# Kernel tuning notes

Measured on AMD Instinct MI355X. Metric: run time of the kernel, lower is better.

Reference implementation:

```python
import jax, jax.numpy as jnp
import numpy as np

# Module hyperparameters (from init_kwargs)
INPUT_SIZE = 1024
OUTPUT_SIZE = 1024
ORDER = 3
GRID_RANGE = (-1.0, 1.0)
GRID_COUNT = 8
CENTER_COUNT = GRID_COUNT + ORDER + 1  # 12

_lo, _hi = GRID_RANGE
_end_center = _hi + (_hi - _lo) * (ORDER + 1) / (GRID_COUNT - 1)
CENTERS = jnp.asarray(np.linspace(_lo, _end_center, CENTER_COUNT), dtype=jnp.float32)
ZOOM = (_hi - _lo) / 2.0
PAN = (_hi + _lo) / 2.0


def setup_inputs() -> dict:
    key = jax.random.key(0)
    k1, k2 = jax.random.split(key)
    x = jax.random.normal(k1, (4096, INPUT_SIZE), dtype=jnp.float32)
    coef = jax.random.normal(k2, (OUTPUT_SIZE, INPUT_SIZE, GRID_COUNT), dtype=jnp.float32) * 0.1
    return {"x": x, "coef": coef}


def _spline_basis(x):
    # x: [B, I] -> basis: [B, I, GRID_COUNT] via Cox-de Boor recursion
    xt = jnp.tanh(x) * ZOOM + PAN
    c = CENTERS
    xe = xt[..., None]  # [B, I, 1]
    # order-0: indicator of [c[i], c[i+1]) for i = 0..CENTER_COUNT-2
    b = ((xe >= c[:-1]) & (xe < c[1:])).astype(xt.dtype)  # [B, I, CENTER_COUNT-1]
    for k in range(1, ORDER + 1):
        n = CENTER_COUNT - k - 1
        c0, ck = c[:n], c[k:k + n]
        c1, ck1 = c[1:n + 1], c[k + 1:k + 1 + n]
        left = (xe - c0) / (ck - c0)          # [B, I, n]
        right = (ck1 - xe) / (ck1 - c1)       # [B, I, n]
        b = left * b[..., :n] + right * b[..., 1:n + 1]
    return b  # [B, I, GRID_COUNT]


def reference(x, coef):
    spline = _spline_basis(x)                      # [B, I, G]
    # sum_j over inputs of coef-weighted basis: [B, O]
    return jnp.einsum('big,oig->bo', spline, coef)
```

## Files before the change

### kernel.cpp

```cpp
#include <hip/hip_runtime.h>
#include <stdint.h>
#include <stddef.h>


#define BATCH 4096
#define IN    1024
#define OUTN  1024
#define KDIM  (IN * 8)
#define NTT   (KDIM / 64)

typedef __attribute__((ext_vector_type(8)))  short          short8;
typedef __attribute__((ext_vector_type(8)))  unsigned short ushort8;
typedef __attribute__((ext_vector_type(4)))  float          f32x4;


__device__ __forceinline__ constexpr float Cf(int i) {
    constexpr double end  = 1.0 + 2.0 * 4.0 / 7.0;
    constexpr double step = (end - (-1.0)) / 11.0;
    return (float)(-1.0 + (double)i * step);
}

__device__ __forceinline__ unsigned short f2bf(float f) {
    unsigned int u = __builtin_bit_cast(unsigned int, f);
    u += 0x7fffu + ((u >> 16) & 1u);
    return (unsigned short)(u >> 16);
}

__device__ __forceinline__ float bf2f(unsigned short u) {
    unsigned int v = (unsigned int)u << 16;
    return __builtin_bit_cast(float, v);
}

__device__ __forceinline__ ushort8 spline8(float xt) {
    float v[11];
#pragma unroll
    for (int j = 0; j < 11; ++j)
        v[j] = (xt >= Cf(j) && xt < Cf(j + 1)) ? 1.0f : 0.0f;
#pragma unroll
    for (int k = 1; k <= 3; ++k) {
#pragma unroll
        for (int j = 0; j < 11 - k; ++j) {
            float left  = (xt - Cf(j))         * (1.0f / (Cf(j + k)     - Cf(j)));
            float right = (Cf(j + k + 1) - xt) * (1.0f / (Cf(j + k + 1) - Cf(j + 1)));
            v[j] = left * v[j] + right * v[j + 1];
        }
    }
    ushort8 r;
#pragma unroll
    for (int g = 0; g < 8; ++g) r[g] = f2bf(v[g]);
    return r;
}

typedef const unsigned int __attribute__((address_space(1))) gu32;
typedef unsigned int       __attribute__((address_space(3))) lu32;

__device__ __forceinline__ void gload_lds16(const void* g, void* l) {
    __builtin_amdgcn_global_load_lds((gu32*)g, (lu32*)l, 16, 0, 0);
}


__global__ void prep_kernel(const float* __restrict__ x, const float* __restrict__ coef,
                            unsigned short* __restrict__ A, unsigned short* __restrict__ B) {
    const int t = threadIdx.x;
    int blk = blockIdx.x;
    if (blk < 4096) {
        const int bb = blk >> 4, bi = blk & 15;
        const int b  = bb * 16 + (t & 15);
        const int i0 = bi * 64 + (t >> 4) * 4;
        f32x4 xv = *reinterpret_cast<const f32x4*>(&x[(size_t)b * IN + i0]);
        ushort8 r[4];
#pragma unroll
        for (int j = 0; j < 4; ++j) r[j] = spline8(tanhf(xv[j]));
        ushort8* out = reinterpret_cast<ushort8*>(A)
                     + ((size_t)(bb * 256 + bi * 16 + (t >> 4)) * 64) + (t & 15);
        out[0]  = r[0];
        out[16] = r[1];
        out[32] = r[2];
        out[48] = r[3];
    } else {
        blk -= 4096;
        const int ob = blk >> 4, ib = blk & 15;
        const int oo = ob * 16 + (t & 15);
        const int i0 = ib * 64 + (t >> 4) * 4;
        const f32x4* cin = reinterpret_cast<const f32x4*>(coef);
        ushort8 r[4];
#pragma unroll
        for (int j = 0; j < 4; ++j) {
            f32x4 v0 = cin[((size_t)oo * IN + i0 + j) * 2];
            f32x4 v1 = cin[((size_t)oo * IN + i0 + j) * 2 + 1];
#pragma unroll
            for (int g = 0; g < 4; ++g) { r[j][g] = f2bf(v0[g]); r[j][4 + g] = f2bf(v1[g]); }
        }
        ushort8* out = reinterpret_cast<ushort8*>(B)
                     + ((size_t)(ob * 256 + ib * 16 + (t >> 4)) * 64) + (t & 15);
        out[0]  = r[0];
        out[16] = r[1];
        out[32] = r[2];
        out[48] = r[3];
    }
}


#define LSA0 (&Ls[0][0])
#define LSB0 (&Ls[0][16384])
#define LSA1 (&Ls[1][0])
#define LSB1 (&Ls[1][16384])

template<int NSPLIT>
__global__ __launch_bounds__(512, 2) void gemm_bt(
        const unsigned short* __restrict__ Ashuf,
        const unsigned short* __restrict__ Bshuf,
        float* __restrict__ C,
        unsigned short* __restrict__ P) {
    constexpr int NT2 = NTT / NSPLIT;
    static_assert((NT2 & 1) == 0, "loop assumes even NT2");
    __shared__ unsigned short Ls[2][32768];

    const int tid  = threadIdx.x;
    const int w    = tid >> 6;
    const int lane = tid & 63;
    const int wm   = w >> 2, wn = w & 3;
    const int kkw  = w & 1, wh = w >> 1;
    const int lane8 = lane * 8;

    const int bid  = blockIdx.x;
    const int s    = bid & (NSPLIT - 1);
    const int tile = bid / NSPLIT;
    const int mb16 = (tile >> 2) * 16;
    const int nb16 = (tile & 3) * 16;
    const int T0   = s * NT2;
    const int brow = mb16 * 16, bcol = nb16 * 16;

#define STAGE_OP(BASE, NB16, H, T, LS) do {                                   \
        size_t _kq = ((size_t)(2 * (T0 + (T)) + kkw)) * 512 + lane8;          \
        const unsigned short* _g = (BASE) + ((size_t)((NB16) + (H)*8 + wh) << 17) + _kq; \
        unsigned short* _l = (LS) + (((H)*16 + w) << 9);                      \
        gload_lds16(_g, _l);                                                  \
        gload_lds16(_g + ((size_t)4 << 17), _l + (8 << 9));                   \
    } while (0)
#define STAGE_A(H, T, LS) STAGE_OP(Ashuf, mb16, H, T, LS)
#define STAGE_B(H, T, LS) STAGE_OP(Bshuf, nb16, H, T, LS)

#define LDA_F(DST, H, LS) do {                                                \
        _Pragma("unroll")                                                     \
        for (int mf = 0; mf < 4; ++mf)                                        \
            _Pragma("unroll")                                                 \
            for (int kk = 0; kk < 2; ++kk)                                    \
                DST[mf][kk] = *reinterpret_cast<const short8*>(               \
                    (LS) + (((((H)*8 + wm*4 + mf) * 2) + kk) << 9) + lane8);  \
    } while (0)
#define LDB_F(DST, V, LS) do {                                                \
        _Pragma("unroll")                                                     \
        for (int nf = 0; nf < 2; ++nf)                                        \
            _Pragma("unroll")                                                 \
            for (int kk = 0; kk < 2; ++kk)                                    \
                DST[nf][kk] = *reinterpret_cast<const short8*>(               \
                    (LS) + (((((V)*8 + wn*2 + nf) * 2) + kk) << 9) + lane8);  \
    } while (0)

    f32x4 acc[8][4] = {};
    short8 aF[4][2], bv0[2][2], bv1[2][2];

#define MFMA_Q(H, V, AF, BV) do {                                             \
        __builtin_amdgcn_s_setprio(1);                                        \
        _Pragma("unroll")                                                     \
        for (int kk = 0; kk < 2; ++kk)                                        \
            _Pragma("unroll")                                                 \
            for (int mf = 0; mf < 4; ++mf)                                    \
                _Pragma("unroll")                                             \
                for (int nf = 0; nf < 2; ++nf)                                \
                    acc[(H)*4 + mf][(V)*2 + nf] =                             \
                        __builtin_amdgcn_mfma_f32_16x16x32_bf16(              \
                            AF[mf][kk], BV[nf][kk],                           \
                            acc[(H)*4 + mf][(V)*2 + nf], 0, 0, 0);            \
        __builtin_amdgcn_s_setprio(0);                                        \
    } while (0)

#define TILE(T, LAC, LBC, LAN, LBN, S1F, S23F, RN, VC) do {                   \
        __builtin_amdgcn_s_barrier();                                         \
        MFMA_Q(0, 0, aF, bv0);                                                \
        LDB_F(bv1, 1, LBC);                                                   \
        if (S1F) { STAGE_B(1, (T) + 1, LBN); STAGE_A(1, (T) + 1, LAN); }      \
        __builtin_amdgcn_s_barrier();                                         \
        MFMA_Q(0, 1, aF, bv1);                                                \
        LDA_F(aF, 1, LAC);                                                    \
        if (S23F) STAGE_B(0, (T) + 2, LBC);                                   \
        __builtin_amdgcn_s_barrier();                                         \
        MFMA_Q(1, 0, aF, bv0);                                                \
        if (S23F) STAGE_A(0, (T) + 2, LAC);                                   \
        asm volatile("s_waitcnt vmcnt(" VC ")" ::: "memory");                 \
        __builtin_amdgcn_s_barrier();                                         \
        MFMA_Q(1, 1, aF, bv1);                                                \
        if (RN) { LDA_F(aF, 0, LAN); LDB_F(bv0, 0, LBN); }                    \
    } while (0)

    STAGE_B(0, 0, LSB0); STAGE_A(0, 0, LSA0);
    STAGE_B(1, 0, LSB0); STAGE_A(1, 0, LSA0);
    STAGE_B(0, 1, LSB1); STAGE_A(0, 1, LSA1);
    asm volatile("s_waitcnt vmcnt(4)" ::: "memory");
    __builtin_amdgcn_s_barrier();
    LDA_F(aF, 0, LSA0); LDB_F(bv0, 0, LSB0);

#pragma unroll 1
    for (int t = 0; t + 2 <= NT2 - 2; t += 2) {
        TILE(t,     LSA0, LSB0, LSA1, LSB1, 1, 1, 1, "4");
        TILE(t + 1, LSA1, LSB1, LSA0, LSB0, 1, 1, 1, "4");
    }
    TILE(NT2 - 2, LSA0, LSB0, LSA1, LSB1, 1, 0, 1, "0");
    TILE(NT2 - 1, LSA1, LSB1, LSA0, LSB0, 0, 0, 0, "0");

    const int q4 = (lane >> 4) * 4, frow = lane & 15;
    if (NSPLIT == 1 || s == 0) {
#pragma unroll
        for (int H = 0; H < 2; ++H)
#pragma unroll
            for (int mf = 0; mf < 4; ++mf)
#pragma unroll
                for (int V = 0; V < 2; ++V)
#pragma unroll
                    for (int nf = 0; nf < 2; ++nf)
#pragma unroll
                        for (int r = 0; r < 4; ++r) {
                            int row = brow + H * 128 + wm * 64 + mf * 16 + q4 + r;
                            int col = bcol + V * 128 + wn * 32 + nf * 16 + frow;
                            C[(size_t)row * OUTN + col] = acc[H * 4 + mf][V * 2 + nf][r];
                        }
    } else {
        unsigned short* Pb = P + (size_t)(s - 1) * BATCH * OUTN;
#pragma unroll
        for (int H = 0; H < 2; ++H)
#pragma unroll
            for (int mf = 0; mf < 4; ++mf)
#pragma unroll
                for (int V = 0; V < 2; ++V)
#pragma unroll
                    for (int nf = 0; nf < 2; ++nf)
#pragma unroll
                        for (int r = 0; r < 4; ++r) {
                            int row = brow + H * 128 + wm * 64 + mf * 16 + q4 + r;
                            int col = bcol + V * 128 + wn * 32 + nf * 16 + frow;
                            Pb[(size_t)row * OUTN + col] = f2bf(acc[H * 4 + mf][V * 2 + nf][r]);
                        }
    }
}


__global__ void reduce_kernel(float* __restrict__ C, const unsigned short* __restrict__ P,
                              int np) {
    int i = blockIdx.x * 256 + threadIdx.x;
    size_t base = (size_t)i * 8;
    f32x4 c0 = *reinterpret_cast<f32x4*>(&C[base]);
    f32x4 c1 = *reinterpret_cast<f32x4*>(&C[base + 4]);
    for (int j = 0; j < np; ++j) {
        ushort8 p = *reinterpret_cast<const ushort8*>(&P[(size_t)j * BATCH * OUTN + base]);
#pragma unroll
        for (int e = 0; e < 4; ++e) c0[e] += bf2f(p[e]);
#pragma unroll
        for (int e = 0; e < 4; ++e) c1[e] += bf2f(p[4 + e]);
    }
    *reinterpret_cast<f32x4*>(&C[base])     = c0;
    *reinterpret_cast<f32x4*>(&C[base + 4]) = c1;
}


extern "C" void kernel_launch(void* const* d_in, const int* in_sizes, int n_in,
                              void* d_out, int out_size, void* d_ws, size_t ws_size,
                              hipStream_t stream) {
    const float* x    = (const float*)d_in[0];
    const float* coef = (const float*)d_in[1];
    float* out = (float*)d_out;

    unsigned short* ashuf = (unsigned short*)d_ws;
    unsigned short* bshuf = ashuf + (size_t)BATCH * KDIM;
    unsigned short* part  = bshuf + (size_t)OUTN * KDIM;
    const size_t base = (size_t)BATCH * KDIM * 2 + (size_t)OUTN * KDIM * 2;
    const size_t slab = (size_t)BATCH * OUTN * 2;

    prep_kernel<<<5120, 256, 0, stream>>>(x, coef, ashuf, bshuf);

    if (ws_size >= base + 3 * slab) {
        gemm_bt<4><<<256, 512, 0, stream>>>(ashuf, bshuf, out, part);
        reduce_kernel<<<2048, 256, 0, stream>>>(out, part, 3);
    } else if (ws_size >= base + slab) {
        gemm_bt<2><<<128, 512, 0, stream>>>(ashuf, bshuf, out, part);
        reduce_kernel<<<2048, 256, 0, stream>>>(out, part, 1);
    } else {
        gemm_bt<1><<<64, 512, 0, stream>>>(ashuf, bshuf, out, nullptr);
    }
}
```

Before: 96.43 us.

## Restructure GEMM to 256-thread blocks with triple-buffered K=32 pipeline

Reworks the bf16 MFMA GEMM so each block is 256 threads computing a 256x128 output tile instead of 512 threads on 256x256. The K loop now advances in 32-wide steps with a three-stage LDS ring buffer, replacing the 64-wide double buffer. This doubles the grid to 512 blocks so more blocks can be resident on the CUs, and it simplifies the staging and barrier schedule. In exchange each block reuses less B data per load and needs more barriers per unit of K. The NSPLIT=2 fallback path is also removed.

```diff
diff --git a/kernel.cpp b/kernel.cpp
--- a/kernel.cpp
+++ b/kernel.cpp
@@ -7,7 +7,7 @@
 #define IN    1024
 #define OUTN  1024
 #define KDIM  (IN * 8)
-#define NTT   (KDIM / 64)
+#define NSTEP (KDIM / 32)
 
 typedef __attribute__((ext_vector_type(8)))  short          short8;
 typedef __attribute__((ext_vector_type(8)))  unsigned short ushort8;
@@ -101,146 +101,135 @@
 }
 
 
-#define LSA0 (&Ls[0][0])
-#define LSB0 (&Ls[0][16384])
-#define LSA1 (&Ls[1][0])
-#define LSB1 (&Ls[1][16384])
-
 template<int NSPLIT>
-__global__ __launch_bounds__(512, 2) void gemm_bt(
+__global__ __launch_bounds__(256, 2) void gemm_bt(
         const unsigned short* __restrict__ Ashuf,
         const unsigned short* __restrict__ Bshuf,
         float* __restrict__ C,
         unsigned short* __restrict__ P) {
-    constexpr int NT2 = NTT / NSPLIT;
-    static_assert((NT2 & 1) == 0, "loop assumes even NT2");
-    __shared__ unsigned short Ls[2][32768];
+    constexpr int NT2 = NSTEP / NSPLIT;
+    static_assert(NT2 >= 8 && (NT2 - 4) % 3 == 0, "tail assumes (NT2-4)%3==0");
+    __shared__ unsigned short Ls[3][12288];
 
     const int tid  = threadIdx.x;
     const int w    = tid >> 6;
     const int lane = tid & 63;
-    const int wm   = w >> 2, wn = w & 3;
-    const int kkw  = w & 1, wh = w >> 1;
+    const int wm   = w >> 1, wn = w & 1;
     const int lane8 = lane * 8;
+    const int w4 = w * 4, w2 = w * 2;
 
     const int bid  = blockIdx.x;
-    const int s    = bid & (NSPLIT - 1);
-    const int tile = bid / NSPLIT;
-    const int mb16 = (tile >> 2) * 16;
-    const int nb16 = (tile & 3) * 16;
+    const int s    = (NSPLIT == 1) ? 0 : (bid & (NSPLIT - 1));
+    const int tile = (NSPLIT == 1) ? bid : (bid / NSPLIT);
+    const int tm   = tile >> 3;
+    const int tn   = tile & 7;
+    const int mb16 = tm * 16;
+    const int nb8  = tn * 8;
     const int T0   = s * NT2;
-    const int brow = mb16 * 16, bcol = nb16 * 16;
-
-#define STAGE_OP(BASE, NB16, H, T, LS) do {                                   \
-        size_t _kq = ((size_t)(2 * (T0 + (T)) + kkw)) * 512 + lane8;          \
-        const unsigned short* _g = (BASE) + ((size_t)((NB16) + (H)*8 + wh) << 17) + _kq; \
-        unsigned short* _l = (LS) + (((H)*16 + w) << 9);                      \
-        gload_lds16(_g, _l);                                                  \
-        gload_lds16(_g + ((size_t)4 << 17), _l + (8 << 9));                   \
-    } while (0)
-#define STAGE_A(H, T, LS) STAGE_OP(Ashuf, mb16, H, T, LS)
-#define STAGE_B(H, T, LS) STAGE_OP(Bshuf, nb16, H, T, LS)
-
-#define LDA_F(DST, H, LS) do {                                                \
+    const int brow = tm * 256, bcol = tn * 128;
+
+#define STAGE(T2, LS) do {                                                    \
+        size_t _kq = (size_t)(T0 + (T2)) * 512 + lane8;                       \
+        _Pragma("unroll")                                                     \
+        for (int j = 0; j < 4; ++j)                                           \
+            gload_lds16(Ashuf + (((size_t)(mb16 + w4 + j)) << 17) + _kq,      \
+                        (LS) + (w4 + j) * 512);                               \
+        _Pragma("unroll")                                                     \
+        for (int j = 0; j < 2; ++j)                                           \
+            gload_lds16(Bshuf + (((size_t)(nb8 + w2 + j)) << 17) + _kq,       \
+                        (LS) + 8192 + (w2 + j) * 512);                        \
+    } while (0)
+
+#define LDA_LO(LS) do {                                                      \
+        _Pragma("unroll")                                                    \
+        for (int mf = 0; mf < 4; ++mf)                                       \
+            aF[mf] = *reinterpret_cast<const short8*>(                       \
+                (LS) + (wm * 8 + mf) * 512 + lane8);                         \
+    } while (0)
+#define LDA_HI(LS) do {                                                     \
+        _Pragma("unroll")                                                    \
+        for (int mf = 0; mf < 4; ++mf)                                       \
+            aF[4 + mf] = *reinterpret_cast<const short8*>(                   \
+                (LS) + (wm * 8 + 4 + mf) * 512 + lane8);                     \
+    } while (0)
+#define LDB(LS) do {                                                         \
+        _Pragma("unroll")                                                    \
+        for (int nf = 0; nf < 4; ++nf)                                       \
+            bv[nf] = *reinterpret_cast<const short8*>(                       \
+                (LS) + 8192 + (wn * 4 + nf) * 512 + lane8);                  \
+    } while (0)
+
+    f32x4 acc[8][4] = {};
+    short8 aF[8], bv[4];
+
+#define MFMA_HALF(L) do {                                                     \
+        __builtin_amdgcn_s_setprio(1);                                        \
         _Pragma("unroll")                                                     \
         for (int mf = 0; mf < 4; ++mf)                                        \
             _Pragma("unroll")                                                 \
-            for (int kk = 0; kk < 2; ++kk)                                    \
-                DST[mf][kk] = *reinterpret_cast<const short8*>(               \
-                    (LS) + (((((H)*8 + wm*4 + mf) * 2) + kk) << 9) + lane8);  \
-    } while (0)
-#define LDB_F(DST, V, LS) do {                                                \
-        _Pragma("unroll")                                                     \
-        for (int nf = 0; nf < 2; ++nf)                                        \
-            _Pragma("unroll")                                                 \
-            for (int kk = 0; kk < 2; ++kk)                                    \
-                DST[nf][kk] = *reinterpret_cast<const short8*>(               \
-                    (LS) + (((((V)*8 + wn*2 + nf) * 2) + kk) << 9) + lane8);  \
-    } while (0)
-
-    f32x4 acc[8][4] = {};
-    short8 aF[4][2], bv0[2][2], bv1[2][2];
-
-#define MFMA_Q(H, V, AF, BV) do {                                             \
-        __builtin_amdgcn_s_setprio(1);                                        \
-        _Pragma("unroll")                                                     \
-        for (int kk = 0; kk < 2; ++kk)                                        \
-            _Pragma("unroll")                                                 \
-            for (int mf = 0; mf < 4; ++mf)                                    \
-                _Pragma("unroll")                                             \
-                for (int nf = 0; nf < 2; ++nf)                                \
-                    acc[(H)*4 + mf][(V)*2 + nf] =                             \
-                        __builtin_amdgcn_mfma_f32_16x16x32_bf16(              \
-                            AF[mf][kk], BV[nf][kk],                           \
-                            acc[(H)*4 + mf][(V)*2 + nf], 0, 0, 0);            \
+            for (int nf = 0; nf < 4; ++nf)                                    \
+                acc[(L)*4 + mf][nf] =                                         \
+                    __builtin_amdgcn_mfma_f32_16x16x32_bf16(                  \
+                        aF[(L)*4 + mf], bv[nf], acc[(L)*4 + mf][nf], 0, 0, 0);\
         __builtin_amdgcn_s_setprio(0);                                        \
     } while (0)
 
-#define TILE(T, LAC, LBC, LAN, LBN, S1F, S23F, RN, VC) do {                   \
+#define STEP(T, CUR, NXT, STG, SFLAG, VC, RN) do {                            \
         __builtin_amdgcn_s_barrier();                                         \
-        MFMA_Q(0, 0, aF, bv0);                                                \
-        LDB_F(bv1, 1, LBC);                                                   \
-        if (S1F) { STAGE_B(1, (T) + 1, LBN); STAGE_A(1, (T) + 1, LAN); }      \
-        __builtin_amdgcn_s_barrier();                                         \
-        MFMA_Q(0, 1, aF, bv1);                                                \
-        LDA_F(aF, 1, LAC);                                                    \
-        if (S23F) STAGE_B(0, (T) + 2, LBC);                                   \
-        __builtin_amdgcn_s_barrier();                                         \
-        MFMA_Q(1, 0, aF, bv0);                                                \
-        if (S23F) STAGE_A(0, (T) + 2, LAC);                                   \
+        if (SFLAG) STAGE((T) + 2, STG);                                       \
+        MFMA_HALF(0);                                                         \
+        LDA_HI(CUR);                                                          \
         asm volatile("s_waitcnt vmcnt(" VC ")" ::: "memory");                 \
         __builtin_amdgcn_s_barrier();                                         \
-        MFMA_Q(1, 1, aF, bv1);                                                \
-        if (RN) { LDA_F(aF, 0, LAN); LDB_F(bv0, 0, LBN); }                    \
-    } while (0)
-
-    STAGE_B(0, 0, LSB0); STAGE_A(0, 0, LSA0);
-    STAGE_B(1, 0, LSB0); STAGE_A(1, 0, LSA0);
-    STAGE_B(0, 1, LSB1); STAGE_A(0, 1, LSA1);
-    asm volatile("s_waitcnt vmcnt(4)" ::: "memory");
+        MFMA_HALF(1);                                                         \
+        if (RN) { LDA_LO(NXT); LDB(NXT); }                                    \
+    } while (0)
+
+    unsigned short* b0 = &Ls[0][0];
+    unsigned short* b1 = &Ls[1][0];
+    unsigned short* b2 = &Ls[2][0];
+
+    STAGE(0, b0);
+    STAGE(1, b1);
+    asm volatile("s_waitcnt vmcnt(6)" ::: "memory");
     __builtin_amdgcn_s_barrier();
-    LDA_F(aF, 0, LSA0); LDB_F(bv0, 0, LSB0);
+    LDA_LO(b0); LDB(b0);
 
 #pragma unroll 1
-    for (int t = 0; t + 2 <= NT2 - 2; t += 2) {
-        TILE(t,     LSA0, LSB0, LSA1, LSB1, 1, 1, 1, "4");
-        TILE(t + 1, LSA1, LSB1, LSA0, LSB0, 1, 1, 1, "4");
-    }
-    TILE(NT2 - 2, LSA0, LSB0, LSA1, LSB1, 1, 0, 1, "0");
-    TILE(NT2 - 1, LSA1, LSB1, LSA0, LSB0, 0, 0, 0, "0");
+    for (int t = 0; t < NT2 - 4; t += 3) {
+        STEP(t,     b0, b1, b2, 1, "6", 1);
+        STEP(t + 1, b1, b2, b0, 1, "6", 1);
+        STEP(t + 2, b2, b0, b1, 1, "6", 1);
+    }
+    STEP(NT2 - 4, b0, b1, b2, 1, "6", 1);
+    STEP(NT2 - 3, b1, b2, b0, 1, "6", 1);
+    STEP(NT2 - 2, b2, b0, b1, 0, "0", 1);
+    STEP(NT2 - 1, b0, b1, b2, 0, "0", 0);
 
     const int q4 = (lane >> 4) * 4, frow = lane & 15;
     if (NSPLIT == 1 || s == 0) {
 #pragma unroll
-        for (int H = 0; H < 2; ++H)
-#pragma unroll
-            for (int mf = 0; mf < 4; ++mf)
-#pragma unroll
-                for (int V = 0; V < 2; ++V)
-#pragma unroll
-                    for (int nf = 0; nf < 2; ++nf)
-#pragma unroll
-                        for (int r = 0; r < 4; ++r) {
-                            int row = brow + H * 128 + wm * 64 + mf * 16 + q4 + r;
-                            int col = bcol + V * 128 + wn * 32 + nf * 16 + frow;
-                            C[(size_t)row * OUTN + col] = acc[H * 4 + mf][V * 2 + nf][r];
-                        }
+        for (int mf = 0; mf < 8; ++mf)
+#pragma unroll
+            for (int nf = 0; nf < 4; ++nf)
+#pragma unroll
+                for (int r = 0; r < 4; ++r) {
+                    int row = brow + wm * 128 + mf * 16 + q4 + r;
+                    int col = bcol + wn * 64 + nf * 16 + frow;
+                    C[(size_t)row * OUTN + col] = acc[mf][nf][r];
+                }
     } else {
         unsigned short* Pb = P + (size_t)(s - 1) * BATCH * OUTN;
 #pragma unroll
-        for (int H = 0; H < 2; ++H)
-#pragma unroll
-            for (int mf = 0; mf < 4; ++mf)
-#pragma unroll
-                for (int V = 0; V < 2; ++V)
-#pragma unroll
-                    for (int nf = 0; nf < 2; ++nf)
-#pragma unroll
-                        for (int r = 0; r < 4; ++r) {
-                            int row = brow + H * 128 + wm * 64 + mf * 16 + q4 + r;
-                            int col = bcol + V * 128 + wn * 32 + nf * 16 + frow;
-                            Pb[(size_t)row * OUTN + col] = f2bf(acc[H * 4 + mf][V * 2 + nf][r]);
-                        }
+        for (int mf = 0; mf < 8; ++mf)
+#pragma unroll
+            for (int nf = 0; nf < 4; ++nf)
+#pragma unroll
+                for (int r = 0; r < 4; ++r) {
+                    int row = brow + wm * 128 + mf * 16 + q4 + r;
+                    int col = bcol + wn * 64 + nf * 16 + frow;
+                    Pb[(size_t)row * OUTN + col] = f2bf(acc[mf][nf][r]);
+                }
     }
 }
 
@@ -279,12 +268,9 @@
     prep_kernel<<<5120, 256, 0, stream>>>(x, coef, ashuf, bshuf);
 
     if (ws_size >= base + 3 * slab) {
-        gemm_bt<4><<<256, 512, 0, stream>>>(ashuf, bshuf, out, part);
+        gemm_bt<4><<<512, 256, 0, stream>>>(ashuf, bshuf, out, part);
         reduce_kernel<<<2048, 256, 0, stream>>>(out, part, 3);
-    } else if (ws_size >= base + slab) {
-        gemm_bt<2><<<128, 512, 0, stream>>>(ashuf, bshuf, out, part);
-        reduce_kernel<<<2048, 256, 0, stream>>>(out, part, 1);
     } else {
-        gemm_bt<1><<<64, 512, 0, stream>>>(ashuf, bshuf, out, nullptr);
-    }
-}
+        gemm_bt<1><<<128, 256, 0, stream>>>(ashuf, bshuf, out, nullptr);
+    }
+}
```

Measured after the change: 101.8 us. +5.6%, slower.

## Load B fragments directly from global memory, stage only A in LDS

Applied to the files above, without the earlier changes.

The GEMM kernel stops staging the B operand through shared memory. Each wave now loads its B fragments straight from global memory into registers, and LDS holds only double-buffered A tiles, halving shared memory use. The pipeline schedule and waitcnt counts are reworked to match. This removes LDS write/read traffic for B and may allow more resident blocks, but B is now fetched redundantly across waves with exposed global latency.

```diff
diff --git a/kernel.cpp b/kernel.cpp
--- a/kernel.cpp
+++ b/kernel.cpp
@@ -102,9 +102,7 @@
 
 
 #define LSA0 (&Ls[0][0])
-#define LSB0 (&Ls[0][16384])
 #define LSA1 (&Ls[1][0])
-#define LSB1 (&Ls[1][16384])
 
 template<int NSPLIT>
 __global__ __launch_bounds__(512, 2) void gemm_bt(
@@ -113,8 +111,8 @@
         float* __restrict__ C,
         unsigned short* __restrict__ P) {
     constexpr int NT2 = NTT / NSPLIT;
-    static_assert((NT2 & 1) == 0, "loop assumes even NT2");
-    __shared__ unsigned short Ls[2][32768];
+    static_assert((NT2 & 1) == 0 && NT2 >= 8, "loop assumes even NT2 >= 8");
+    __shared__ unsigned short Ls[2][16384];
 
     const int tid  = threadIdx.x;
     const int w    = tid >> 6;
@@ -131,15 +129,13 @@
     const int T0   = s * NT2;
     const int brow = mb16 * 16, bcol = nb16 * 16;
 
-#define STAGE_OP(BASE, NB16, H, T, LS) do {                                   \
+#define STAGE_A(H, T, LS) do {                                                \
         size_t _kq = ((size_t)(2 * (T0 + (T)) + kkw)) * 512 + lane8;          \
-        const unsigned short* _g = (BASE) + ((size_t)((NB16) + (H)*8 + wh) << 17) + _kq; \
+        const unsigned short* _g = Ashuf + ((size_t)(mb16 + (H)*8 + wh) << 17) + _kq; \
         unsigned short* _l = (LS) + (((H)*16 + w) << 9);                      \
         gload_lds16(_g, _l);                                                  \
         gload_lds16(_g + ((size_t)4 << 17), _l + (8 << 9));                   \
     } while (0)
-#define STAGE_A(H, T, LS) STAGE_OP(Ashuf, mb16, H, T, LS)
-#define STAGE_B(H, T, LS) STAGE_OP(Bshuf, nb16, H, T, LS)
 
 #define LDA_F(DST, H, LS) do {                                                \
         _Pragma("unroll")                                                     \
@@ -149,13 +145,16 @@
                 DST[mf][kk] = *reinterpret_cast<const short8*>(               \
                     (LS) + (((((H)*8 + wm*4 + mf) * 2) + kk) << 9) + lane8);  \
     } while (0)
-#define LDB_F(DST, V, LS) do {                                                \
+
+#define LOADB(DST, T, V) do {                                                 \
+        size_t _kb = (size_t)(2 * (T0 + (T))) * 512 + lane8;                  \
         _Pragma("unroll")                                                     \
         for (int nf = 0; nf < 2; ++nf)                                        \
             _Pragma("unroll")                                                 \
             for (int kk = 0; kk < 2; ++kk)                                    \
                 DST[nf][kk] = *reinterpret_cast<const short8*>(               \
-                    (LS) + (((((V)*8 + wn*2 + nf) * 2) + kk) << 9) + lane8);  \
+                    Bshuf + (((size_t)(nb16 + (V)*8 + wn*2 + nf)) << 17)      \
+                          + _kb + (size_t)kk * 512);                          \
     } while (0)
 
     f32x4 acc[8][4] = {};
@@ -176,38 +175,39 @@
         __builtin_amdgcn_s_setprio(0);                                        \
     } while (0)
 
-#define TILE(T, LAC, LBC, LAN, LBN, S1F, S23F, RN, VC) do {                   \
+#define TILE(T, LC, LN, SFLAG, BFLAG, VC, RN) do {                            \
         __builtin_amdgcn_s_barrier();                                         \
         MFMA_Q(0, 0, aF, bv0);                                                \
-        LDB_F(bv1, 1, LBC);                                                   \
-        if (S1F) { STAGE_B(1, (T) + 1, LBN); STAGE_A(1, (T) + 1, LAN); }      \
-        __builtin_amdgcn_s_barrier();                                         \
+        asm volatile("s_waitcnt vmcnt(" VC ")" ::: "memory");                 \
+        __builtin_amdgcn_s_barrier();                                         \
+        if (SFLAG) STAGE_A(0, (T) + 2, LC);                                   \
         MFMA_Q(0, 1, aF, bv1);                                                \
-        LDA_F(aF, 1, LAC);                                                    \
-        if (S23F) STAGE_B(0, (T) + 2, LBC);                                   \
+        LDA_F(aF, 1, LC);                                                     \
         __builtin_amdgcn_s_barrier();                                         \
         MFMA_Q(1, 0, aF, bv0);                                                \
-        if (S23F) STAGE_A(0, (T) + 2, LAC);                                   \
+        if (BFLAG) LOADB(bv0, (T) + 1, 0);                                    \
         asm volatile("s_waitcnt vmcnt(" VC ")" ::: "memory");                 \
         __builtin_amdgcn_s_barrier();                                         \
+        if (SFLAG) STAGE_A(1, (T) + 2, LC);                                   \
         MFMA_Q(1, 1, aF, bv1);                                                \
-        if (RN) { LDA_F(aF, 0, LAN); LDB_F(bv0, 0, LBN); }                    \
-    } while (0)
-
-    STAGE_B(0, 0, LSB0); STAGE_A(0, 0, LSA0);
-    STAGE_B(1, 0, LSB0); STAGE_A(1, 0, LSA0);
-    STAGE_B(0, 1, LSB1); STAGE_A(0, 1, LSA1);
-    asm volatile("s_waitcnt vmcnt(4)" ::: "memory");
+        if (RN) LDA_F(aF, 0, LN);                                             \
+        if (BFLAG) LOADB(bv1, (T) + 1, 1);                                    \
+    } while (0)
+
+    STAGE_A(0, 0, LSA0); STAGE_A(1, 0, LSA0);
+    STAGE_A(0, 1, LSA1); STAGE_A(1, 1, LSA1);
+    LOADB(bv0, 0, 0); LOADB(bv1, 0, 1);
+    asm volatile("s_waitcnt vmcnt(12)" ::: "memory");
     __builtin_amdgcn_s_barrier();
-    LDA_F(aF, 0, LSA0); LDB_F(bv0, 0, LSB0);
+    LDA_F(aF, 0, LSA0);
 
 #pragma unroll 1
     for (int t = 0; t + 2 <= NT2 - 2; t += 2) {
-        TILE(t,     LSA0, LSB0, LSA1, LSB1, 1, 1, 1, "4");
-        TILE(t + 1, LSA1, LSB1, LSA0, LSB0, 1, 1, 1, "4");
-    }
-    TILE(NT2 - 2, LSA0, LSB0, LSA1, LSB1, 1, 0, 1, "0");
-    TILE(NT2 - 1, LSA1, LSB1, LSA0, LSB0, 0, 0, 0, "0");
+        TILE(t,     LSA0, LSA1, 1, 1, "4", 1);
+        TILE(t + 1, LSA1, LSA0, 1, 1, "4", 1);
+    }
+    TILE(NT2 - 2, LSA0, LSA1, 0, 1, "0", 1);
+    TILE(NT2 - 1, LSA1, LSA0, 0, 0, "0", 0);
 
     const int q4 = (lane >> 4) * 4, frow = lane & 15;
     if (NSPLIT == 1 || s == 0) {
```

After: 102.0 us. 1.06x slower.

## Switch GEMM to 32x32x16 bf16 MFMA with matching fragment layout

Applied to the files above, without the earlier changes.

Replaces the 16x16x32 bf16 MFMA tiles with 32x32x16 MFMA instructions. The prep kernel's shuffled A/B layout, the LDS staging addresses and the fragment loads are reorganised into 32-row fragments. Each instruction now does more work per operand load, which cuts the number of LDS fragment reads and MFMA issues per tile. In exchange, the accumulator output mapping and epilogue become more complex, and register pressure may change.

```diff
diff --git a/kernel.cpp b/kernel.cpp
--- a/kernel.cpp
+++ b/kernel.cpp
@@ -12,6 +12,7 @@
 typedef __attribute__((ext_vector_type(8)))  short          short8;
 typedef __attribute__((ext_vector_type(8)))  unsigned short ushort8;
 typedef __attribute__((ext_vector_type(4)))  float          f32x4;
+typedef __attribute__((ext_vector_type(16))) float          f32x16;
 
 
 __device__ __forceinline__ constexpr float Cf(int i) {
@@ -64,39 +65,41 @@
     const int t = threadIdx.x;
     int blk = blockIdx.x;
     if (blk < 4096) {
-        const int bb = blk >> 4, bi = blk & 15;
-        const int b  = bb * 16 + (t & 15);
-        const int i0 = bi * 64 + (t >> 4) * 4;
-        f32x4 xv = *reinterpret_cast<const f32x4*>(&x[(size_t)b * IN + i0]);
+        const int rb = blk >> 5, ib = blk & 31;
+        const int row = rb * 32 + (t & 31);
+        const int i0  = ib * 32 + (t >> 5) * 4;
+        f32x4 xv = *reinterpret_cast<const f32x4*>(&x[(size_t)row * IN + i0]);
         ushort8 r[4];
 #pragma unroll
         for (int j = 0; j < 4; ++j) r[j] = spline8(tanhf(xv[j]));
+        const int kb0 = ib * 16 + (t >> 5) * 2;
         ushort8* out = reinterpret_cast<ushort8*>(A)
-                     + ((size_t)(bb * 256 + bi * 16 + (t >> 4)) * 64) + (t & 15);
+                     + ((size_t)rb * 512 + kb0) * 64 + (t & 31);
         out[0]  = r[0];
-        out[16] = r[1];
-        out[32] = r[2];
-        out[48] = r[3];
+        out[32] = r[1];
+        out[64] = r[2];
+        out[96] = r[3];
     } else {
         blk -= 4096;
-        const int ob = blk >> 4, ib = blk & 15;
-        const int oo = ob * 16 + (t & 15);
-        const int i0 = ib * 64 + (t >> 4) * 4;
+        const int ob = blk >> 5, ibk = blk & 31;
+        const int o  = ob * 32 + (t & 31);
+        const int i0 = ibk * 32 + (t >> 5) * 4;
         const f32x4* cin = reinterpret_cast<const f32x4*>(coef);
         ushort8 r[4];
 #pragma unroll
         for (int j = 0; j < 4; ++j) {
-            f32x4 v0 = cin[((size_t)oo * IN + i0 + j) * 2];
-            f32x4 v1 = cin[((size_t)oo * IN + i0 + j) * 2 + 1];
+            f32x4 v0 = cin[((size_t)o * IN + i0 + j) * 2];
+            f32x4 v1 = cin[((size_t)o * IN + i0 + j) * 2 + 1];
 #pragma unroll
             for (int g = 0; g < 4; ++g) { r[j][g] = f2bf(v0[g]); r[j][4 + g] = f2bf(v1[g]); }
         }
+        const int kb0 = ibk * 16 + (t >> 5) * 2;
         ushort8* out = reinterpret_cast<ushort8*>(B)
-                     + ((size_t)(ob * 256 + ib * 16 + (t >> 4)) * 64) + (t & 15);
+                     + ((size_t)ob * 512 + kb0) * 64 + (t & 31);
         out[0]  = r[0];
-        out[16] = r[1];
-        out[32] = r[2];
-        out[48] = r[3];
+        out[32] = r[1];
+        out[64] = r[2];
+        out[96] = r[3];
     }
 }
 
@@ -113,85 +116,82 @@
         float* __restrict__ C,
         unsigned short* __restrict__ P) {
     constexpr int NT2 = NTT / NSPLIT;
-    static_assert((NT2 & 1) == 0, "loop assumes even NT2");
+    static_assert((NT2 & 1) == 0 && NT2 >= 8, "loop assumes even NT2 >= 8");
     __shared__ unsigned short Ls[2][32768];
 
     const int tid  = threadIdx.x;
     const int w    = tid >> 6;
     const int lane = tid & 63;
     const int wm   = w >> 2, wn = w & 3;
-    const int kkw  = w & 1, wh = w >> 1;
     const int lane8 = lane * 8;
 
     const int bid  = blockIdx.x;
     const int s    = bid & (NSPLIT - 1);
     const int tile = bid / NSPLIT;
-    const int mb16 = (tile >> 2) * 16;
-    const int nb16 = (tile & 3) * 16;
+    const int tm   = tile >> 2, tn = tile & 3;
+    const int mb8  = tm * 8;
+    const int nb8  = tn * 8;
     const int T0   = s * NT2;
-    const int brow = mb16 * 16, bcol = nb16 * 16;
-
-#define STAGE_OP(BASE, NB16, H, T, LS) do {                                   \
-        size_t _kq = ((size_t)(2 * (T0 + (T)) + kkw)) * 512 + lane8;          \
-        const unsigned short* _g = (BASE) + ((size_t)((NB16) + (H)*8 + wh) << 17) + _kq; \
-        unsigned short* _l = (LS) + (((H)*16 + w) << 9);                      \
+    const int brow = tm * 256, bcol = tn * 256;
+
+#define STAGE_OP(BASE, NB, H, T, LS) do {                                     \
+        const int _f   = (H) * 4 + (w >> 1);                                  \
+        const int _kbl = (w & 1) * 2;                                         \
+        const unsigned short* _g = (BASE) + ((size_t)((NB) + _f) << 18)       \
+                  + ((size_t)((T0 + (T)) * 4 + _kbl) << 9) + lane8;           \
+        unsigned short* _l = (LS) + ((_f * 4 + _kbl) << 9);                   \
         gload_lds16(_g, _l);                                                  \
-        gload_lds16(_g + ((size_t)4 << 17), _l + (8 << 9));                   \
-    } while (0)
-#define STAGE_A(H, T, LS) STAGE_OP(Ashuf, mb16, H, T, LS)
-#define STAGE_B(H, T, LS) STAGE_OP(Bshuf, nb16, H, T, LS)
-
-#define LDA_F(DST, H, LS) do {                                                \
+        gload_lds16(_g + 512, _l + 512);                                      \
+    } while (0)
+#define STAGE_A(H, T, LS) STAGE_OP(Ashuf, mb8, H, T, LS)
+#define STAGE_B(H, T, LS) STAGE_OP(Bshuf, nb8, H, T, LS)
+
+#define LDA_HF(H, LS) do {                                                    \
         _Pragma("unroll")                                                     \
-        for (int mf = 0; mf < 4; ++mf)                                        \
+        for (int mf2 = 0; mf2 < 2; ++mf2)                                     \
             _Pragma("unroll")                                                 \
-            for (int kk = 0; kk < 2; ++kk)                                    \
-                DST[mf][kk] = *reinterpret_cast<const short8*>(               \
-                    (LS) + (((((H)*8 + wm*4 + mf) * 2) + kk) << 9) + lane8);  \
-    } while (0)
-#define LDB_F(DST, V, LS) do {                                                \
+            for (int k = 0; k < 4; ++k)                                       \
+                aF[mf2][k] = *reinterpret_cast<const short8*>(                \
+                    (LS) + ((((H)*4 + wm*2 + mf2) * 4 + k) << 9) + lane8);    \
+    } while (0)
+#define LDB_V(DST, V, LS) do {                                                \
         _Pragma("unroll")                                                     \
-        for (int nf = 0; nf < 2; ++nf)                                        \
-            _Pragma("unroll")                                                 \
-            for (int kk = 0; kk < 2; ++kk)                                    \
-                DST[nf][kk] = *reinterpret_cast<const short8*>(               \
-                    (LS) + (((((V)*8 + wn*2 + nf) * 2) + kk) << 9) + lane8);  \
-    } while (0)
-
-    f32x4 acc[8][4] = {};
-    short8 aF[4][2], bv0[2][2], bv1[2][2];
-
-#define MFMA_Q(H, V, AF, BV) do {                                             \
+        for (int k = 0; k < 4; ++k)                                           \
+            DST[k] = *reinterpret_cast<const short8*>(                        \
+                (LS) + ((((V)*4 + wn) * 4 + k) << 9) + lane8);                \
+    } while (0)
+
+    f32x16 acc[4][2] = {};
+    short8 aF[2][4], bv0[4], bv1[4];
+
+#define MFMA_W(H, V, BV) do {                                                 \
         __builtin_amdgcn_s_setprio(1);                                        \
         _Pragma("unroll")                                                     \
-        for (int kk = 0; kk < 2; ++kk)                                        \
+        for (int k = 0; k < 4; ++k)                                           \
             _Pragma("unroll")                                                 \
-            for (int mf = 0; mf < 4; ++mf)                                    \
-                _Pragma("unroll")                                             \
-                for (int nf = 0; nf < 2; ++nf)                                \
-                    acc[(H)*4 + mf][(V)*2 + nf] =                             \
-                        __builtin_amdgcn_mfma_f32_16x16x32_bf16(              \
-                            AF[mf][kk], BV[nf][kk],                           \
-                            acc[(H)*4 + mf][(V)*2 + nf], 0, 0, 0);            \
+            for (int mf2 = 0; mf2 < 2; ++mf2)                                 \
+                acc[(H)*2 + mf2][V] =                                         \
+                    __builtin_amdgcn_mfma_f32_32x32x16_bf16(                  \
+                        aF[mf2][k], BV[k], acc[(H)*2 + mf2][V], 0, 0, 0);     \
         __builtin_amdgcn_s_setprio(0);                                        \
     } while (0)
 
 #define TILE(T, LAC, LBC, LAN, LBN, S1F, S23F, RN, VC) do {                   \
         __builtin_amdgcn_s_barrier();                                         \
-        MFMA_Q(0, 0, aF, bv0);                                                \
-        LDB_F(bv1, 1, LBC);                                                   \
+        MFMA_W(0, 0, bv0);                                                    \
+        LDB_V(bv1, 1, LBC);                                                   \
         if (S1F) { STAGE_B(1, (T) + 1, LBN); STAGE_A(1, (T) + 1, LAN); }      \
         __builtin_amdgcn_s_barrier();                                         \
-        MFMA_Q(0, 1, aF, bv1);                                                \
-        LDA_F(aF, 1, LAC);                                                    \
+        MFMA_W(0, 1, bv1);                                                    \
+        LDA_HF(1, LAC);                                                       \
         if (S23F) STAGE_B(0, (T) + 2, LBC);                                   \
         __builtin_amdgcn_s_barrier();                                         \
-        MFMA_Q(1, 0, aF, bv0);                                                \
+        MFMA_W(1, 0, bv0);                                                    \
         if (S23F) STAGE_A(0, (T) + 2, LAC);                                   \
         asm volatile("s_waitcnt vmcnt(" VC ")" ::: "memory");                 \
         __builtin_amdgcn_s_barrier();                                         \
-        MFMA_Q(1, 1, aF, bv1);                                                \
-        if (RN) { LDA_F(aF, 0, LAN); LDB_F(bv0, 0, LBN); }                    \
+        MFMA_W(1, 1, bv1);                                                    \
+        if (RN) { LDA_HF(0, LAN); LDB_V(bv0, 0, LBN); }                       \
     } while (0)
 
     STAGE_B(0, 0, LSB0); STAGE_A(0, 0, LSA0);
@@ -199,7 +199,7 @@
     STAGE_B(0, 1, LSB1); STAGE_A(0, 1, LSA1);
     asm volatile("s_waitcnt vmcnt(4)" ::: "memory");
     __builtin_amdgcn_s_barrier();
-    LDA_F(aF, 0, LSA0); LDB_F(bv0, 0, LSB0);
+    LDA_HF(0, LSA0); LDB_V(bv0, 0, LSB0);
 
 #pragma unroll 1
     for (int t = 0; t + 2 <= NT2 - 2; t += 2) {
@@ -209,38 +209,36 @@
     TILE(NT2 - 2, LSA0, LSB0, LSA1, LSB1, 1, 0, 1, "0");
     TILE(NT2 - 1, LSA1, LSB1, LSA0, LSB0, 0, 0, 0, "0");
 
-    const int q4 = (lane >> 4) * 4, frow = lane & 15;
+    const int rbase = 4 * (lane >> 5), fcol = lane & 31;
     if (NSPLIT == 1 || s == 0) {
 #pragma unroll
         for (int H = 0; H < 2; ++H)
 #pragma unroll
-            for (int mf = 0; mf < 4; ++mf)
+            for (int mf2 = 0; mf2 < 2; ++mf2)
 #pragma unroll
                 for (int V = 0; V < 2; ++V)
 #pragma unroll
-                    for (int nf = 0; nf < 2; ++nf)
-#pragma unroll
-                        for (int r = 0; r < 4; ++r) {
-                            int row = brow + H * 128 + wm * 64 + mf * 16 + q4 + r;
-                            int col = bcol + V * 128 + wn * 32 + nf * 16 + frow;
-                            C[(size_t)row * OUTN + col] = acc[H * 4 + mf][V * 2 + nf][r];
-                        }
+                    for (int r = 0; r < 16; ++r) {
+                        int row = brow + H * 128 + wm * 64 + mf2 * 32
+                                + (r & 3) + 8 * (r >> 2) + rbase;
+                        int col = bcol + V * 128 + wn * 32 + fcol;
+                        C[(size_t)row * OUTN + col] = acc[H * 2 + mf2][V][r];
+                    }
     } else {
         unsigned short* Pb = P + (size_t)(s - 1) * BATCH * OUTN;
 #pragma unroll
         for (int H = 0; H < 2; ++H)
 #pragma unroll
-            for (int mf = 0; mf < 4; ++mf)
+            for (int mf2 = 0; mf2 < 2; ++mf2)
 #pragma unroll
                 for (int V = 0; V < 2; ++V)
 #pragma unroll
-                    for (int nf = 0; nf < 2; ++nf)
-#pragma unroll
-                        for (int r = 0; r < 4; ++r) {
-                            int row = brow + H * 128 + wm * 64 + mf * 16 + q4 + r;
-                            int col = bcol + V * 128 + wn * 32 + nf * 16 + frow;
-                            Pb[(size_t)row * OUTN + col] = f2bf(acc[H * 4 + mf][V * 2 + nf][r]);
-                        }
+                    for (int r = 0; r < 16; ++r) {
+                        int row = brow + H * 128 + wm * 64 + mf2 * 32
+                                + (r & 3) + 8 * (r >> 2) + rbase;
+                        int col = bcol + V * 128 + wn * 32 + fcol;
+                        Pb[(size_t)row * OUTN + col] = f2bf(acc[H * 2 + mf2][V][r]);
+                    }
     }
 }
 
```

Result: slower. 103.5 us (+7.3%).
